# Optimization experiments

Hardware: AMD Instinct MI355X
Metric: run time of the kernel (lower is better)

## Reference

```python
import jax, jax.numpy as jnp
import numpy as np

D_MODEL = 512
NUM_HEADS = 8
NUM_SIGNALS = 8
HEAD_DIM = D_MODEL // NUM_HEADS          # 64
D_H = HEAD_DIM // NUM_SIGNALS            # 8
LN_EPS = 1e-5


def setup_inputs() -> dict:
    key = jax.random.key(0)
    ks = jax.random.split(key, 8)
    B, N, C = 2, 2048, D_MODEL
    s = 1.0 / np.sqrt(C)
    return {
        "x": jax.random.normal(ks[0], (B, N, C), dtype=jnp.float32),
        "mask": jax.random.randint(ks[1], (B, N), 0, 2, dtype=jnp.int32),
        "ln_g": jnp.ones((C,), dtype=jnp.float32),
        "ln_b": jnp.zeros((C,), dtype=jnp.float32),
        "wq": jax.random.normal(ks[2], (C, C), dtype=jnp.float32) * s,
        "bq": jnp.zeros((C,), dtype=jnp.float32),
        "wk": jax.random.normal(ks[3], (C, C), dtype=jnp.float32) * s,
        "bk": jnp.zeros((C,), dtype=jnp.float32),
        "wv": jax.random.normal(ks[4], (C, C), dtype=jnp.float32) * s,
        "bv": jnp.zeros((C,), dtype=jnp.float32),
        "wo": jax.random.normal(ks[5], (C, C), dtype=jnp.float32) * s,
        "bo": jnp.zeros((C,), dtype=jnp.float32),
    }


def reference(x, mask, ln_g, ln_b, wq, bq, wk, bk, wv, bv, wo, bo):
    B, N, C = x.shape
    H, S, dh, hd = NUM_HEADS, NUM_SIGNALS, D_H, HEAD_DIM
    # LayerNorm
    mu = jnp.mean(x, axis=-1, keepdims=True)
    var = jnp.mean(jnp.square(x - mu), axis=-1, keepdims=True)
    xn = (x - mu) * jax.lax.rsqrt(var + LN_EPS) * ln_g + ln_b
    # Projections (torch Linear: y = x @ W.T + b; here weights are stored (in,out))
    q = (xn @ wq + bq).reshape(B, N, H, hd).transpose(0, 2, 1, 3)  # (B,H,N,hd)
    k = (xn @ wk + bk).reshape(B, N, H, hd).transpose(0, 2, 1, 3)
    v = (xn @ wv + bv).reshape(B, N, H, hd).transpose(0, 2, 1, 3)
    # mean over S signals of q_s k_s^T / sqrt(d_h) == full-head contraction / (S*sqrt(d_h))
    scale = 1.0 / (S * np.sqrt(dh))
    avg_logits = jnp.einsum("bhnd,bhmd->bhnm", q, k) * scale  # (B,H,N,N)
    # key-padding mask: (B,N) -> (B,1,1,N)
    avg_logits = jnp.where(mask[:, None, None, :] == 0, -10000.0, avg_logits)
    attn = jax.nn.softmax(avg_logits, axis=-1)
    attn = jnp.nan_to_num(attn)
    out = jnp.einsum("bhnm,bhmd->bhnd", attn, v)  # (B,H,N,hd)
    out = out.transpose(0, 2, 1, 3).reshape(B, N, C)
    return out @ wo + bo
```

## Files before the change

### kernel.cpp

```cpp
#include <hip/hip_runtime.h>
#include <math.h>

#define SEQ_N 2048
#define BATCH 2
#define CDIM 512
#define NHEADS 8
#define MROWS (BATCH * SEQ_N)
#define QKV_N 1536
#define KSPLIT 1536
#define ATTN_SCALE 0.044194173824159216f

typedef __attribute__((ext_vector_type(8))) __bf16 bf16x8;
typedef __attribute__((ext_vector_type(4))) float  f32x4;

static __device__ __forceinline__ unsigned short f2bf(float f) {
    __bf16 h = (__bf16)f;
    return __builtin_bit_cast(unsigned short, h);
}
static __device__ __forceinline__ float bf2f(unsigned short u) {
    return (float)__builtin_bit_cast(__bf16, u);
}

static __device__ __forceinline__ void gll16(const void* g, void* l) {
    __builtin_amdgcn_global_load_lds(
        (const __attribute__((address_space(1))) unsigned int*)g,
        (__attribute__((address_space(3))) unsigned int*)l, 16, 0, 0);
}

__global__ __launch_bounds__(128) void ln_split_kernel(
    const float* __restrict__ x, const float* __restrict__ g,
    const float* __restrict__ bta,
    unsigned short* __restrict__ xn_hi, unsigned short* __restrict__ xn_lo)
{
    int row = blockIdx.x;
    int t = threadIdx.x;
    const float4* xr = (const float4*)(x + (size_t)row * CDIM);
    float4 v = xr[t];
    float s  = v.x + v.y + v.z + v.w;
    float ss = v.x*v.x + v.y*v.y + v.z*v.z + v.w*v.w;
    #pragma unroll
    for (int off = 1; off <= 32; off <<= 1) {
        s  += __shfl_xor(s,  off);
        ss += __shfl_xor(ss, off);
    }
    __shared__ float red[4];
    if ((t & 63) == 0) { red[(t >> 6) * 2] = s; red[(t >> 6) * 2 + 1] = ss; }
    __syncthreads();
    s  = red[0] + red[2];
    ss = red[1] + red[3];
    float mean = s * (1.0f / CDIM);
    float var  = ss * (1.0f / CDIM) - mean * mean;
    float rstd = rsqrtf(var + 1e-5f);
    float4 gv = ((const float4*)g)[t];
    float4 bv = ((const float4*)bta)[t];
    float o[4];
    o[0] = (v.x - mean) * rstd * gv.x + bv.x;
    o[1] = (v.y - mean) * rstd * gv.y + bv.y;
    o[2] = (v.z - mean) * rstd * gv.z + bv.z;
    o[3] = (v.w - mean) * rstd * gv.w + bv.w;
    unsigned int ph[2], pl[2];
    #pragma unroll
    for (int i = 0; i < 2; ++i) {
        unsigned short h0 = f2bf(o[2*i]);
        unsigned short h1 = f2bf(o[2*i+1]);
        unsigned short l0 = f2bf(o[2*i]   - bf2f(h0));
        unsigned short l1 = f2bf(o[2*i+1] - bf2f(h1));
        ph[i] = (unsigned int)h0 | ((unsigned int)h1 << 16);
        pl[i] = (unsigned int)l0 | ((unsigned int)l1 << 16);
    }
    *(uint2*)&xn_hi[(size_t)row * CDIM + t * 4] = make_uint2(ph[0], ph[1]);
    *(uint2*)&xn_lo[(size_t)row * CDIM + t * 4] = make_uint2(pl[0], pl[1]);
}

__global__ __launch_bounds__(256) void wsplit_kernel(
    const float* __restrict__ wq, const float* __restrict__ wk,
    const float* __restrict__ wv, const float* __restrict__ wo,
    unsigned short* __restrict__ BTqkv, unsigned short* __restrict__ BTo)
{
    int m = blockIdx.z;
    const float* W = (m == 0) ? wq : (m == 1) ? wk : (m == 2) ? wv : wo;
    int k0 = blockIdx.y * 64, c0 = blockIdx.x * 64;
    __shared__ float tile[64][68];
    int t = threadIdx.x;
    int r = t >> 4, ch = t & 15;
    #pragma unroll
    for (int i = 0; i < 4; ++i) {
        float4 v = *(const float4*)&W[(size_t)(k0 + r + i*16) * CDIM + c0 + ch*4];
        tile[r + i*16][ch*4 + 0] = v.x; tile[r + i*16][ch*4 + 1] = v.y;
        tile[r + i*16][ch*4 + 2] = v.z; tile[r + i*16][ch*4 + 3] = v.w;
    }
    __syncthreads();
    unsigned short* BT = (m < 3) ? BTqkv : BTo;
    int nbase = (m < 3) ? m * CDIM : 0;
    #pragma unroll
    for (int i = 0; i < 4; ++i) {
        int c  = c0 + r + i*16;
        int kk = k0 + ch*4;
        unsigned int hi2[2], lo2[2];
        #pragma unroll
        for (int half = 0; half < 2; ++half) {
            unsigned short h[2], l[2];
            #pragma unroll
            for (int j = 0; j < 2; ++j) {
                float v = tile[ch*4 + half*2 + j][r + i*16];
                h[j] = f2bf(v);
                l[j] = f2bf(v - bf2f(h[j]));
            }
            hi2[half] = (unsigned int)h[0] | ((unsigned int)h[1] << 16);
            lo2[half] = (unsigned int)l[0] | ((unsigned int)l[1] << 16);
        }
        size_t ro = (size_t)(nbase + c) * KSPLIT;
        *(uint2*)&BT[ro + kk]        = make_uint2(hi2[0], hi2[1]);
        *(uint2*)&BT[ro + 512 + kk]  = make_uint2(lo2[0], lo2[1]);
        *(uint2*)&BT[ro + 1024 + kk] = make_uint2(hi2[0], hi2[1]);
    }
}

__global__ __launch_bounds__(256) void gemm_split_kernel(
    const unsigned short* __restrict__ Ahi, const unsigned short* __restrict__ Alo,
    const unsigned short* __restrict__ BT,
    const float* __restrict__ b0, const float* __restrict__ b1,
    const float* __restrict__ b2,
    unsigned short* __restrict__ outb, float* __restrict__ outf)
{
    __shared__ unsigned short As[128 * 64];
    __shared__ unsigned short Bs[64 * 64];
    int tid = threadIdx.x;
    int l = tid & 63, w = tid >> 6;
    int am = w >> 1, an = w & 1;
    int m0 = blockIdx.y * 128, n0 = blockIdx.x * 64;

    f32x4 acc[4][2];
    #pragma unroll
    for (int fm = 0; fm < 4; ++fm)
        #pragma unroll
        for (int fn = 0; fn < 2; ++fn)
            acc[fm][fn] = (f32x4){0.f, 0.f, 0.f, 0.f};

    for (int kt = 0; kt < 24; ++kt) {
        int kp  = kt * 64;
        int seg = kp >> 9;
        const unsigned short* Asrc = (seg < 2) ? Ahi : Alo;
        int ac0 = kp & 511;
        __syncthreads();
        #pragma unroll
        for (int i = 0; i < 4; ++i) {
            int c = tid + i * 256;
            int row = c >> 3, c8 = c & 7;
            gll16(Asrc + (size_t)(m0 + row) * CDIM + ac0 + c8 * 8, &As[c * 8]);
        }
        #pragma unroll
        for (int i = 0; i < 2; ++i) {
            int c = tid + i * 256;
            int row = c >> 3, c8 = c & 7;
            gll16(BT + (size_t)(n0 + row) * KSPLIT + kp + c8 * 8, &Bs[c * 8]);
        }
        __syncthreads();
        #pragma unroll
        for (int kc = 0; kc < 2; ++kc) {
            bf16x8 af[4], bfr[2];
            #pragma unroll
            for (int fm = 0; fm < 4; ++fm)
                af[fm] = *(const bf16x8*)&As[(am*64 + fm*16 + (l & 15)) * 64 + kc*32 + (l >> 4) * 8];
            #pragma unroll
            for (int fn = 0; fn < 2; ++fn)
                bfr[fn] = *(const bf16x8*)&Bs[(an*32 + fn*16 + (l & 15)) * 64 + kc*32 + (l >> 4) * 8];
            #pragma unroll
            for (int fm = 0; fm < 4; ++fm)
                #pragma unroll
                for (int fn = 0; fn < 2; ++fn)
                    acc[fm][fn] = __builtin_amdgcn_mfma_f32_16x16x32_bf16(
                        af[fm], bfr[fn], acc[fm][fn], 0, 0, 0);
        }
    }
    #pragma unroll
    for (int fm = 0; fm < 4; ++fm)
        #pragma unroll
        for (int fn = 0; fn < 2; ++fn)
            #pragma unroll
            for (int r = 0; r < 4; ++r) {
                int row = m0 + am*64 + fm*16 + (l >> 4) * 4 + r;
                int col = n0 + an*32 + fn*16 + (l & 15);
                float v = acc[fm][fn][r];
                if (outb) {
                    float bias = (col < 512) ? b0[col]
                               : (col < 1024) ? b1[col - 512] : b2[col - 1024];
                    outb[(size_t)row * QKV_N + col] = f2bf(v + bias);
                } else {
                    outf[(size_t)row * CDIM + col] = v + b0[col];
                }
            }
}

__global__ __launch_bounds__(256) void attn_kernel(
    const unsigned short* __restrict__ qkv, const int* __restrict__ maskp,
    unsigned short* __restrict__ ao_hi, unsigned short* __restrict__ ao_lo)
{
    __shared__ unsigned short Ks[64 * 72];
    __shared__ unsigned short VTs[64 * 72];
    __shared__ unsigned short Ps[4][16 * 72];
    __shared__ float mskf[64];

    int tid = threadIdx.x, l = tid & 63, w = tid >> 6;
    int bh = blockIdx.x;
    int b = bh >> 3, head = bh & 7;
    int q0 = blockIdx.y * 64;
    size_t brow = (size_t)b * SEQ_N;
    const unsigned short* Qb = qkv + head * 64;
    const unsigned short* Kb = qkv + 512 + head * 64;
    const unsigned short* Vb = qkv + 1024 + head * 64;

    bf16x8 qf[2];
    {
        int qrow = q0 + w * 16 + (l & 15);
        #pragma unroll
        for (int kc = 0; kc < 2; ++kc)
            qf[kc] = *(const bf16x8*)&Qb[(brow + qrow) * QKV_N + kc*32 + (l >> 4) * 8];
    }

    float m_i[4], l_i[4];
    f32x4 o[4];
    #pragma unroll
    for (int r = 0; r < 4; ++r) { m_i[r] = -1e30f; l_i[r] = 0.f; }
    #pragma unroll
    for (int nb = 0; nb < 4; ++nb) o[nb] = (f32x4){0.f, 0.f, 0.f, 0.f};

    for (int kv0 = 0; kv0 < SEQ_N; kv0 += 64) {
        __syncthreads();
        #pragma unroll
        for (int i = 0; i < 2; ++i) {
            int c = tid + i * 256;
            int row = c >> 3, c8 = c & 7;
            *(uint4*)&Ks[row * 72 + c8 * 8] =
                *(const uint4*)&Kb[(brow + kv0 + row) * QKV_N + c8 * 8];
        }
        #pragma unroll
        for (int i = 0; i < 2; ++i) {
            int c = tid + i * 256;
            int row = c >> 3, c8 = c & 7;
            uint4 vv = *(const uint4*)&Vb[(brow + kv0 + row) * QKV_N + c8 * 8];
            const unsigned short* pv = (const unsigned short*)&vv;
            int swc = ((row >> 3) ^ c8) & 7;
            #pragma unroll
            for (int j = 0; j < 8; ++j)
                VTs[(c8 * 8 + j) * 72 + swc * 8 + (row & 7)] = pv[j];
        }
        if (tid < 64) mskf[tid] = (float)maskp[b * SEQ_N + kv0 + tid];
        __syncthreads();

        f32x4 s[4];
        #pragma unroll
        for (int nb = 0; nb < 4; ++nb) s[nb] = (f32x4){0.f, 0.f, 0.f, 0.f};
        #pragma unroll
        for (int kc = 0; kc < 2; ++kc)
            #pragma unroll
            for (int nb = 0; nb < 4; ++nb) {
                bf16x8 kf = *(const bf16x8*)&Ks[(nb*16 + (l & 15)) * 72 + kc*32 + (l >> 4) * 8];
                s[nb] = __builtin_amdgcn_mfma_f32_16x16x32_bf16(qf[kc], kf, s[nb], 0, 0, 0);
            }

        #pragma unroll
        for (int nb = 0; nb < 4; ++nb) {
            float mk = mskf[nb * 16 + (l & 15)];
            #pragma unroll
            for (int r = 0; r < 4; ++r)
                s[nb][r] = (mk != 0.f) ? s[nb][r] * ATTN_SCALE : -10000.f;
        }

        #pragma unroll
        for (int r = 0; r < 4; ++r) {
            float rm = fmaxf(fmaxf(s[0][r], s[1][r]), fmaxf(s[2][r], s[3][r]));
            #pragma unroll
            for (int off = 1; off < 16; off <<= 1)
                rm = fmaxf(rm, __shfl_xor(rm, off));
            float mnew  = fmaxf(m_i[r], rm);
            float alpha = __expf(m_i[r] - mnew);
            float p[4], rs = 0.f;
            #pragma unroll
            for (int nb = 0; nb < 4; ++nb) { p[nb] = __expf(s[nb][r] - mnew); rs += p[nb]; }
            #pragma unroll
            for (int off = 1; off < 16; off <<= 1)
                rs += __shfl_xor(rs, off);
            l_i[r] = l_i[r] * alpha + rs;
            m_i[r] = mnew;
            #pragma unroll
            for (int nb = 0; nb < 4; ++nb) o[nb][r] *= alpha;
            int prow = (l >> 4) * 4 + r;
            #pragma unroll
            for (int nb = 0; nb < 4; ++nb)
                Ps[w][prow * 72 + nb * 16 + (l & 15)] = f2bf(p[nb]);
        }

        #pragma unroll
        for (int kc = 0; kc < 2; ++kc) {
            bf16x8 pf = *(const bf16x8*)&Ps[w][(l & 15) * 72 + kc*32 + (l >> 4) * 8];
            int kb = kc * 4 + (l >> 4);
            #pragma unroll
            for (int nb = 0; nb < 4; ++nb) {
                int d = nb * 16 + (l & 15);
                bf16x8 vf = *(const bf16x8*)&VTs[d * 72 + ((kb ^ (d >> 3)) & 7) * 8];
                o[nb] = __builtin_amdgcn_mfma_f32_16x16x32_bf16(pf, vf, o[nb], 0, 0, 0);
            }
        }
    }

    #pragma unroll
    for (int r = 0; r < 4; ++r) {
        float invl = 1.f / l_i[r];
        int row = q0 + w * 16 + (l >> 4) * 4 + r;
        #pragma unroll
        for (int nb = 0; nb < 4; ++nb) {
            float v = o[nb][r] * invl;
            unsigned short h  = f2bf(v);
            unsigned short lo = f2bf(v - bf2f(h));
            size_t idx = (brow + row) * (size_t)CDIM + head * 64 + nb * 16 + (l & 15);
            ao_hi[idx] = h;
            ao_lo[idx] = lo;
        }
    }
}

extern "C" void kernel_launch(void* const* d_in, const int* in_sizes, int n_in,
                              void* d_out, int out_size, void* d_ws, size_t ws_size,
                              hipStream_t stream) {
    const float* x    = (const float*)d_in[0];
    const int*   mask = (const int*)  d_in[1];
    const float* ln_g = (const float*)d_in[2];
    const float* ln_b = (const float*)d_in[3];
    const float* wq   = (const float*)d_in[4];
    const float* bq   = (const float*)d_in[5];
    const float* wk   = (const float*)d_in[6];
    const float* bk   = (const float*)d_in[7];
    const float* wv   = (const float*)d_in[8];
    const float* bv   = (const float*)d_in[9];
    const float* wo   = (const float*)d_in[10];
    const float* bo   = (const float*)d_in[11];
    float* out = (float*)d_out;

    unsigned short* xn_hi = (unsigned short*)d_ws;
    unsigned short* xn_lo = xn_hi + (size_t)MROWS * CDIM;
    unsigned short* BTqkv = xn_lo + (size_t)MROWS * CDIM;
    unsigned short* BTo   = BTqkv + (size_t)QKV_N * KSPLIT;
    unsigned short* qkvb  = BTo   + (size_t)CDIM * KSPLIT;
    unsigned short* ao_hi = qkvb  + (size_t)MROWS * QKV_N;
    unsigned short* ao_lo = ao_hi + (size_t)MROWS * CDIM;

    ln_split_kernel<<<MROWS, 128, 0, stream>>>(x, ln_g, ln_b, xn_hi, xn_lo);
    wsplit_kernel<<<dim3(8, 8, 4), 256, 0, stream>>>(wq, wk, wv, wo, BTqkv, BTo);

    gemm_split_kernel<<<dim3(QKV_N / 64, MROWS / 128), 256, 0, stream>>>(
        xn_hi, xn_lo, BTqkv, bq, bk, bv, qkvb, nullptr);

    attn_kernel<<<dim3(BATCH * NHEADS, SEQ_N / 64), 256, 0, stream>>>(
        qkvb, mask, ao_hi, ao_lo);

    gemm_split_kernel<<<dim3(CDIM / 64, MROWS / 128), 256, 0, stream>>>(
        ao_hi, ao_lo, BTo, bo, nullptr, nullptr, nullptr, out);
}
```

Measured before the change: 250.6 us.

## Split attention over KV chunks with combine kernel; widen QKV GEMM tile

Attention is split along the key/value sequence into up to 4 partitions, each writing unnormalized partial outputs plus row max and sum to workspace. A new combine kernel merges them with log-sum-exp rescaling and emits the hi/lo bf16 split. This targets low occupancy in the original grid of 512 blocks. The QKV projection GEMM also moves to 128-wide N tiles with 512 threads, which gives fewer, larger blocks. The cost is an extra fp32 round trip through memory, one more kernel launch, and dependence on workspace size.

```diff
diff --git a/kernel.cpp b/kernel.cpp
--- a/kernel.cpp
+++ b/kernel.cpp
@@ -9,6 +9,8 @@
 #define QKV_N 1536
 #define KSPLIT 1536
 #define ATTN_SCALE 0.044194173824159216f
+#define BH (BATCH * NHEADS)
+#define ROWS_ALL (BH * SEQ_N)
 
 typedef __attribute__((ext_vector_type(8))) __bf16 bf16x8;
 typedef __attribute__((ext_vector_type(4))) float  f32x4;
@@ -116,19 +118,24 @@
     }
 }
 
-__global__ __launch_bounds__(256) void gemm_split_kernel(
+template<int BN>
+__global__ __launch_bounds__(BN == 128 ? 512 : 256) void gemm_split_kernel(
     const unsigned short* __restrict__ Ahi, const unsigned short* __restrict__ Alo,
     const unsigned short* __restrict__ BT,
     const float* __restrict__ b0, const float* __restrict__ b1,
     const float* __restrict__ b2,
     unsigned short* __restrict__ outb, float* __restrict__ outf)
 {
+    constexpr int NT  = (BN == 128) ? 512 : 256;
+    constexpr int ACH = 1024 / NT;
+    constexpr int BCH = (BN * 8) / NT;
     __shared__ unsigned short As[128 * 64];
-    __shared__ unsigned short Bs[64 * 64];
+    __shared__ unsigned short Bs[BN * 64];
     int tid = threadIdx.x;
     int l = tid & 63, w = tid >> 6;
-    int am = w >> 1, an = w & 1;
-    int m0 = blockIdx.y * 128, n0 = blockIdx.x * 64;
+    int am = (BN == 128) ? (w >> 2) : (w >> 1);
+    int an = (BN == 128) ? (w & 3)  : (w & 1);
+    int m0 = blockIdx.y * 128, n0 = blockIdx.x * BN;
 
     f32x4 acc[4][2];
     #pragma unroll
@@ -144,14 +151,14 @@
         int ac0 = kp & 511;
         __syncthreads();
         #pragma unroll
-        for (int i = 0; i < 4; ++i) {
-            int c = tid + i * 256;
+        for (int i = 0; i < ACH; ++i) {
+            int c = tid + i * NT;
             int row = c >> 3, c8 = c & 7;
             gll16(Asrc + (size_t)(m0 + row) * CDIM + ac0 + c8 * 8, &As[c * 8]);
         }
         #pragma unroll
-        for (int i = 0; i < 2; ++i) {
-            int c = tid + i * 256;
+        for (int i = 0; i < BCH; ++i) {
+            int c = tid + i * NT;
             int row = c >> 3, c8 = c & 7;
             gll16(BT + (size_t)(n0 + row) * KSPLIT + kp + c8 * 8, &Bs[c * 8]);
         }
@@ -194,6 +201,7 @@
 
 __global__ __launch_bounds__(256) void attn_kernel(
     const unsigned short* __restrict__ qkv, const int* __restrict__ maskp,
+    float* __restrict__ Opart, float* __restrict__ mpart, float* __restrict__ lpart,
     unsigned short* __restrict__ ao_hi, unsigned short* __restrict__ ao_lo)
 {
     __shared__ unsigned short Ks[64 * 72];
@@ -205,6 +213,8 @@
     int bh = blockIdx.x;
     int b = bh >> 3, head = bh & 7;
     int q0 = blockIdx.y * 64;
+    int kvlen = SEQ_N / gridDim.z;
+    int kvbeg = blockIdx.z * kvlen;
     size_t brow = (size_t)b * SEQ_N;
     const unsigned short* Qb = qkv + head * 64;
     const unsigned short* Kb = qkv + 512 + head * 64;
@@ -225,7 +235,7 @@
     #pragma unroll
     for (int nb = 0; nb < 4; ++nb) o[nb] = (f32x4){0.f, 0.f, 0.f, 0.f};
 
-    for (int kv0 = 0; kv0 < SEQ_N; kv0 += 64) {
+    for (int kv0 = kvbeg; kv0 < kvbeg + kvlen; kv0 += 64) {
         __syncthreads();
         #pragma unroll
         for (int i = 0; i < 2; ++i) {
@@ -304,20 +314,74 @@
         }
     }
 
-    #pragma unroll
-    for (int r = 0; r < 4; ++r) {
-        float invl = 1.f / l_i[r];
-        int row = q0 + w * 16 + (l >> 4) * 4 + r;
-        #pragma unroll
-        for (int nb = 0; nb < 4; ++nb) {
-            float v = o[nb][r] * invl;
-            unsigned short h  = f2bf(v);
-            unsigned short lo = f2bf(v - bf2f(h));
-            size_t idx = (brow + row) * (size_t)CDIM + head * 64 + nb * 16 + (l & 15);
-            ao_hi[idx] = h;
-            ao_lo[idx] = lo;
-        }
-    }
+    if (Opart) {
+        int part = blockIdx.z * BH + bh;
+        #pragma unroll
+        for (int r = 0; r < 4; ++r) {
+            int row = q0 + w * 16 + (l >> 4) * 4 + r;
+            size_t rbase = ((size_t)part * SEQ_N + row) * 64;
+            #pragma unroll
+            for (int nb = 0; nb < 4; ++nb)
+                Opart[rbase + nb * 16 + (l & 15)] = o[nb][r];
+            if ((l & 15) == 0) {
+                mpart[(size_t)part * SEQ_N + row] = m_i[r];
+                lpart[(size_t)part * SEQ_N + row] = l_i[r];
+            }
+        }
+    } else {
+        #pragma unroll
+        for (int r = 0; r < 4; ++r) {
+            float invl = 1.f / l_i[r];
+            int row = q0 + w * 16 + (l >> 4) * 4 + r;
+            #pragma unroll
+            for (int nb = 0; nb < 4; ++nb) {
+                float v = o[nb][r] * invl;
+                unsigned short h  = f2bf(v);
+                unsigned short lo = f2bf(v - bf2f(h));
+                size_t idx = (brow + row) * (size_t)CDIM + head * 64 + nb * 16 + (l & 15);
+                ao_hi[idx] = h;
+                ao_lo[idx] = lo;
+            }
+        }
+    }
+}
+
+__global__ __launch_bounds__(256) void combine_kernel(
+    const float* __restrict__ Opart, const float* __restrict__ mpart,
+    const float* __restrict__ lpart, int S,
+    unsigned short* __restrict__ ao_hi, unsigned short* __restrict__ ao_lo)
+{
+    int t = threadIdx.x;
+    int row = blockIdx.x * 32 + (t >> 3);
+    int d0 = (t & 7) * 8;
+    float ms = -3.0e38f;
+    for (int s = 0; s < S; ++s)
+        ms = fmaxf(ms, mpart[(size_t)s * ROWS_ALL + row]);
+    float L = 0.f;
+    float acc[8] = {0.f,0.f,0.f,0.f,0.f,0.f,0.f,0.f};
+    for (int s = 0; s < S; ++s) {
+        float wgt = __expf(mpart[(size_t)s * ROWS_ALL + row] - ms);
+        L = fmaf(lpart[(size_t)s * ROWS_ALL + row], wgt, L);
+        const float4* op = (const float4*)&Opart[((size_t)s * ROWS_ALL + row) * 64 + d0];
+        float4 a = op[0], c = op[1];
+        acc[0] = fmaf(a.x, wgt, acc[0]); acc[1] = fmaf(a.y, wgt, acc[1]);
+        acc[2] = fmaf(a.z, wgt, acc[2]); acc[3] = fmaf(a.w, wgt, acc[3]);
+        acc[4] = fmaf(c.x, wgt, acc[4]); acc[5] = fmaf(c.y, wgt, acc[5]);
+        acc[6] = fmaf(c.z, wgt, acc[6]); acc[7] = fmaf(c.w, wgt, acc[7]);
+    }
+    float inv = 1.f / L;
+    int bh = row >> 11, n = row & 2047;
+    int b = bh >> 3, h = bh & 7;
+    size_t oidx = ((size_t)(b * SEQ_N + n)) * CDIM + h * 64 + d0;
+    unsigned short hs[8], ls[8];
+    #pragma unroll
+    for (int j = 0; j < 8; ++j) {
+        float v = acc[j] * inv;
+        hs[j] = f2bf(v);
+        ls[j] = f2bf(v - bf2f(hs[j]));
+    }
+    *(uint4*)&ao_hi[oidx] = *(uint4*)hs;
+    *(uint4*)&ao_lo[oidx] = *(uint4*)ls;
 }
 
 extern "C" void kernel_launch(void* const* d_in, const int* in_sizes, int n_in,
@@ -344,16 +408,34 @@
     unsigned short* qkvb  = BTo   + (size_t)CDIM * KSPLIT;
     unsigned short* ao_hi = qkvb  + (size_t)MROWS * QKV_N;
     unsigned short* ao_lo = ao_hi + (size_t)MROWS * CDIM;
+    unsigned short* ws_end = ao_lo + (size_t)MROWS * CDIM;
+
+    size_t base_bytes = (size_t)((char*)ws_end - (char*)d_ws);
+    const size_t part_bytes = (size_t)ROWS_ALL * (64 + 2) * 4;
+    int S = 1;
+    if (base_bytes + 4 * part_bytes <= ws_size) S = 4;
+    else if (base_bytes + 2 * part_bytes <= ws_size) S = 2;
+
+    float* Opart = (float*)ws_end;
+    float* mpart = Opart + (size_t)S * ROWS_ALL * 64;
+    float* lpart = mpart + (size_t)S * ROWS_ALL;
 
     ln_split_kernel<<<MROWS, 128, 0, stream>>>(x, ln_g, ln_b, xn_hi, xn_lo);
     wsplit_kernel<<<dim3(8, 8, 4), 256, 0, stream>>>(wq, wk, wv, wo, BTqkv, BTo);
 
-    gemm_split_kernel<<<dim3(QKV_N / 64, MROWS / 128), 256, 0, stream>>>(
+    gemm_split_kernel<128><<<dim3(QKV_N / 128, MROWS / 128), 512, 0, stream>>>(
         xn_hi, xn_lo, BTqkv, bq, bk, bv, qkvb, nullptr);
 
-    attn_kernel<<<dim3(BATCH * NHEADS, SEQ_N / 64), 256, 0, stream>>>(
-        qkvb, mask, ao_hi, ao_lo);
-
-    gemm_split_kernel<<<dim3(CDIM / 64, MROWS / 128), 256, 0, stream>>>(
+    if (S > 1) {
+        attn_kernel<<<dim3(BH, SEQ_N / 64, S), 256, 0, stream>>>(
+            qkvb, mask, Opart, mpart, lpart, nullptr, nullptr);
+        combine_kernel<<<ROWS_ALL / 32, 256, 0, stream>>>(
+            Opart, mpart, lpart, S, ao_hi, ao_lo);
+    } else {
+        attn_kernel<<<dim3(BH, SEQ_N / 64, 1), 256, 0, stream>>>(
+            qkvb, mask, nullptr, nullptr, nullptr, ao_hi, ao_lo);
+    }
+
+    gemm_split_kernel<64><<<dim3(CDIM / 64, MROWS / 128), 256, 0, stream>>>(
         ao_hi, ao_lo, BTo, bo, nullptr, nullptr, nullptr, out);
 }
```

Result: faster. 244.4 us (-2.5%).
